# Optimization experiments

Measured on AMD Instinct MI355X. Metric: run time of the kernel, lower is better.

## Reference

```python
import jax, jax.numpy as jnp
import numpy as np


def _round_ste(v):
    # straight-through rounding (typical LinearQuantize autograd STE)
    return v + jax.lax.stop_gradient(jnp.round(v) - v)


def setup_inputs() -> dict:
    key = jax.random.key(0)
    k1, k2, k3 = jax.random.split(key, 3)
    tokens, d_in, d_out = 8192, 2048, 2048
    x = jax.random.uniform(k1, (tokens, d_in), dtype=jnp.float32)  # non-negative acts
    weight = jax.random.normal(k2, (d_out, d_in), dtype=jnp.float32) * 0.02
    bias = jax.random.normal(k3, (d_out,), dtype=jnp.float32) * 0.02
    return {"x": x, "weight": weight, "bias": bias, "weight_bit": 8}


def reference(x, weight, bias, weight_bit):
    n = 2 ** weight_bit
    # stats computed on detached data (x.data/w.data in torch)
    wd = jax.lax.stop_gradient(weight)
    w_min = wd.min(axis=1)                      # [out]
    w_max = wd.max(axis=1)                      # [out]
    x_max = jax.lax.stop_gradient(x).max()
    scale_x = (n - 1) / jnp.clip(x_max, 1e-8)
    # activation quantization: round(scale_x * x - 0)
    q_x = _round_ste(scale_x * x)               # [T, in]
    # per-channel asymmetric weight quant (quantize_int)
    scale_w = (n - 1) / jnp.clip(w_max - w_min, 1e-8)   # [out]
    zp_w = scale_w * w_min                      # [out]
    q_w = _round_ste(scale_w[:, None] * weight - zp_w[:, None])  # [out, in]
    # bias quantized with combined scale, then clamped
    q_b = jnp.clip(_round_ste(bias * scale_w * scale_x), -n - 1, n)  # [out]
    # fake-int GEMM + zero-point correction + rescale
    mult = jnp.einsum('ti,oi->to', q_x, q_w) + q_b      # [T, out]
    res = mult + zp_w * q_x.sum(-1, keepdims=True)
    return res / scale_x / scale_w
```

## Files before the change

### kernel.cpp

```cpp
#include <hip/hip_runtime.h>
#include <stdint.h>

typedef __attribute__((ext_vector_type(4))) int i32x4;

__device__ inline float wave_max(float v){ for(int o=32;o;o>>=1) v=fmaxf(v,__shfl_xor(v,o)); return v; }
__device__ inline float wave_min(float v){ for(int o=32;o;o>>=1) v=fminf(v,__shfl_xor(v,o)); return v; }
__device__ inline int   wave_sum(int v){ for(int o=32;o;o>>=1) v+=__shfl_xor(v,o); return v; }

__device__ inline void gload16(const void* g, void* l){
  __builtin_amdgcn_global_load_lds((const __attribute__((address_space(1))) char*)g,
                                   (__attribute__((address_space(3))) char*)l, 16, 0, 0);
}

__global__ void k_xmax_partial(const float* __restrict__ x, long long n4,
                               float* __restrict__ partials){
  long long i = (long long)blockIdx.x*blockDim.x + threadIdx.x;
  long long stride = (long long)gridDim.x*blockDim.x;
  const float4* x4 = (const float4*)x;
  float m = 0.f;
  for(; i < n4; i += stride){
    float4 v = x4[i];
    m = fmaxf(m, fmaxf(fmaxf(v.x,v.y),fmaxf(v.z,v.w)));
  }
  m = wave_max(m);
  __shared__ float sm[4];
  int lane = threadIdx.x & 63, wid = threadIdx.x >> 6;
  if(lane==0) sm[wid] = m;
  __syncthreads();
  if(threadIdx.x==0)
    partials[blockIdx.x] = fmaxf(fmaxf(sm[0],sm[1]),fmaxf(sm[2],sm[3]));
}

__global__ void k_xmax_final(const float* __restrict__ partials, int nPart,
                             uint32_t* __restrict__ xmax_bits){
  float m = 0.f;
  for(int i = threadIdx.x; i < nPart; i += 256) m = fmaxf(m, partials[i]);
  m = wave_max(m);
  __shared__ float sm[4];
  int lane = threadIdx.x & 63, wid = threadIdx.x >> 6;
  if(lane==0) sm[wid] = m;
  __syncthreads();
  if(threadIdx.x==0)
    *xmax_bits = __float_as_uint(fmaxf(fmaxf(sm[0],sm[1]),fmaxf(sm[2],sm[3])));
}

__global__ void k_wstat(const float* __restrict__ w, const float* __restrict__ bias,
                        const int* __restrict__ wbit, const uint32_t* __restrict__ xmax_bits,
                        float* __restrict__ scale_w, float* __restrict__ zp_w,
                        float* __restrict__ winv,
                        int* __restrict__ cint, char* __restrict__ qw, int din){
  int row = blockIdx.x, tid = threadIdx.x;
  int lane = tid & 63, wid = tid >> 6;
  const float4* wr4 = (const float4*)(w + (long long)row*din);
  float4 a = wr4[tid*2], b = wr4[tid*2+1];
  float v[8] = {a.x,a.y,a.z,a.w,b.x,b.y,b.z,b.w};
  float mn = v[0], mx = v[0];
  for(int j=1;j<8;j++){ mn=fminf(mn,v[j]); mx=fmaxf(mx,v[j]); }
  float wmn = wave_min(mn), wmx = wave_max(mx);
  __shared__ float smn[4], smx[4];
  __shared__ float s_sw, s_zp; __shared__ int s_qb;
  if(lane==0){ smn[wid]=wmn; smx[wid]=wmx; }
  __syncthreads();
  if(tid==0){
    float fmn = fminf(fminf(smn[0],smn[1]),fminf(smn[2],smn[3]));
    float fmx = fmaxf(fmaxf(smx[0],smx[1]),fmaxf(smx[2],smx[3]));
    int n = 1 << *wbit;
    float nm1 = (float)(n-1);
    float xmax = __uint_as_float(*xmax_bits);
    float sx = __fdiv_rn(nm1, fmaxf(xmax, 1e-8f));
    float rng = __fsub_rn(fmx, fmn);
    float rngc = fmaxf(rng, 1e-8f);
    float sw = __fdiv_rn(nm1, rngc);
    float zp = __fmul_rn(sw, fmn);
    float qbf = rintf(__fmul_rn(__fmul_rn(bias[row], sw), sx));
    qbf = fminf(fmaxf(qbf, -(float)(n+1)), (float)n);
    s_sw = sw; s_zp = zp; s_qb = (int)qbf;
    scale_w[row] = sw; zp_w[row] = zp;
    winv[row] = __fdiv_rn(rngc, nm1);
  }
  __syncthreads();
  float sw = s_sw, zp = s_zp;
  int qsum = 0; uint32_t lo = 0, hi = 0;
  for(int j=0;j<8;j++){
    int q = (int)rintf(__fsub_rn(__fmul_rn(sw, v[j]), zp));
    qsum += q;
    uint32_t u = (uint32_t)((q - 128) & 0xff);
    if(j<4) lo |= u << (8*j); else hi |= u << (8*(j-4));
  }
  uint32_t* qrow = (uint32_t*)(qw + (long long)row*din);
  qrow[tid*2] = lo; qrow[tid*2+1] = hi;
  int wsum = wave_sum(qsum);
  __shared__ int ssum[4];
  if(lane==0) ssum[wid] = wsum;
  __syncthreads();
  if(tid==0){
    int Sb = ssum[0]+ssum[1]+ssum[2]+ssum[3];
    cint[row] = 128*Sb - 128*128*din + s_qb;
  }
}

__global__ void k_xquant(const float* __restrict__ x, const int* __restrict__ wbit,
                         const uint32_t* __restrict__ xmax_bits,
                         char* __restrict__ qx, int* __restrict__ Sa, int din){
  int row = blockIdx.x, tid = threadIdx.x;
  int lane = tid & 63, wid = tid >> 6;
  int n = 1 << *wbit;
  float nm1 = (float)(n-1);
  float sx = __fdiv_rn(nm1, fmaxf(__uint_as_float(*xmax_bits), 1e-8f));
  const float4* xr4 = (const float4*)(x + (long long)row*din);
  float4 a = xr4[tid*2], b = xr4[tid*2+1];
  float v[8] = {a.x,a.y,a.z,a.w,b.x,b.y,b.z,b.w};
  int qsum = 0; uint32_t lo = 0, hi = 0;
  for(int j=0;j<8;j++){
    int q = (int)rintf(__fmul_rn(sx, v[j]));
    qsum += q;
    uint32_t u = (uint32_t)((q - 128) & 0xff);
    if(j<4) lo |= u << (8*j); else hi |= u << (8*(j-4));
  }
  uint32_t* qrow = (uint32_t*)(qx + (long long)row*din);
  qrow[tid*2] = lo; qrow[tid*2+1] = hi;
  int wsum = wave_sum(qsum);
  __shared__ int ssum[4];
  if(lane==0) ssum[wid] = wsum;
  __syncthreads();
  if(tid==0) Sa[row] = ssum[0]+ssum[1]+ssum[2]+ssum[3];
}

#define ASLOT 16384
#define BSLOT 8192
#define SLOT  (ASLOT + BSLOT)

__global__ __launch_bounds__(256, 2) void k_gemm(
    const char* __restrict__ qx, const char* __restrict__ qw,
    const int* __restrict__ Sa, const int* __restrict__ cint,
    const float* __restrict__ winv, const float* __restrict__ zp_w,
    const int* __restrict__ wbit, const uint32_t* __restrict__ xmax_bits,
    float* __restrict__ out, int T, int dout, int din){
  extern __shared__ char lds[];
  const int tid = threadIdx.x, lane = tid & 63, wid = tid >> 6;
  const int wr = (wid >> 1) * 128, wc = (wid & 1) * 64;
  const int tileN = blockIdx.x, tileM = blockIdx.y;

  const int rbase = tid >> 2, c2 = tid & 3;
  const char* aG[4]; const char* bG[2]; int ldA[4], ldB[2];
  #pragma unroll
  for(int j=0;j<4;j++){
    int row = j*64 + rbase;
    int sc = c2 ^ ((row >> 1) & 3);
    aG[j] = qx + ((long long)tileM*256 + row)*din + sc*16;
    ldA[j] = (j*256 + tid)*16;
  }
  #pragma unroll
  for(int j=0;j<2;j++){
    int row = j*64 + rbase;
    int sc = c2 ^ ((row >> 1) & 3);
    bG[j] = qw + ((long long)tileN*128 + row)*din + sc*16;
    ldB[j] = ASLOT + (j*256 + tid)*16;
  }

  const int physo = (((lane >> 4) ^ ((lane >> 1) & 3)) * 16);
  const int arowL = wr + (lane & 15);
  const int browL = wc + (lane & 15);

  i32x4 acc[8][4] = {};
  const int nk = din / 64;

  {
    char* s0 = lds; char* s1 = lds + SLOT;
    #pragma unroll
    for(int j=0;j<4;j++) gload16(aG[j], s0 + ldA[j]);
    #pragma unroll
    for(int j=0;j<2;j++) gload16(bG[j], s0 + ldB[j]);
    #pragma unroll
    for(int j=0;j<4;j++) gload16(aG[j] + 64, s1 + ldA[j]);
    #pragma unroll
    for(int j=0;j<2;j++) gload16(bG[j] + 64, s1 + ldB[j]);
  }
  asm volatile("s_waitcnt vmcnt(6)" ::: "memory");
  __builtin_amdgcn_s_barrier();

  for(int kt = 0; kt < nk; ++kt){
    char* As = lds + (kt % 3)*SLOT;
    char* Bs = As + ASLOT;

    if(kt + 2 < nk){
      char* Sn = lds + ((kt + 2) % 3)*SLOT;
      const long long ko = (long long)(kt + 2) * 64;
      #pragma unroll
      for(int j=0;j<4;j++) gload16(aG[j] + ko, Sn + ldA[j]);
      #pragma unroll
      for(int j=0;j<2;j++) gload16(bG[j] + ko, Sn + ldB[j]);
    }

    i32x4 bf[4], af[8];
    #pragma unroll
    for(int ni=0; ni<4; ++ni) bf[ni] = *(const i32x4*)(Bs + (browL + ni*16)*64 + physo);
    #pragma unroll
    for(int mi=0; mi<8; ++mi) af[mi] = *(const i32x4*)(As + (arowL + mi*16)*64 + physo);

    __builtin_amdgcn_s_setprio(1);
    #pragma unroll
    for(int mi=0; mi<8; ++mi)
      #pragma unroll
      for(int ni=0; ni<4; ++ni)
        acc[mi][ni] = __builtin_amdgcn_mfma_i32_16x16x64_i8(af[mi], bf[ni], acc[mi][ni], 0, 0, 0);
    __builtin_amdgcn_s_setprio(0);

    if(kt < nk - 2) asm volatile("s_waitcnt vmcnt(6)" ::: "memory");
    else            asm volatile("s_waitcnt vmcnt(0)" ::: "memory");
    __builtin_amdgcn_s_barrier();
  }

  const float nm1 = (float)((1 << *wbit) - 1);
  const float xmaxc = fmaxf(__uint_as_float(*xmax_bits), 1e-8f);
  const float inv_sx = __fdiv_rn(xmaxc, nm1);
  const int colL = tileN*128 + wc + (lane & 15);
  const int rowL = tileM*256 + wr + ((lane >> 4) * 4);
  float invc[4], zp4[4]; int ci4[4];
  #pragma unroll
  for(int ni=0; ni<4; ++ni){
    int o = colL + ni*16;
    invc[ni] = __fmul_rn(winv[o], inv_sx);
    zp4[ni]  = zp_w[o];
    ci4[ni]  = cint[o];
  }
  #pragma unroll
  for(int mi=0; mi<8; ++mi){
    int rb = rowL + mi*16;
    int sav[4];
    #pragma unroll
    for(int r=0; r<4; ++r) sav[r] = Sa[rb + r];
    #pragma unroll
    for(int ni=0; ni<4; ++ni){
      #pragma unroll
      for(int r=0; r<4; ++r){
        int iv = acc[mi][ni][r] + 128*sav[r] + ci4[ni];
        float f = (float)iv + zp4[ni]*(float)sav[r];
        out[(long long)(rb + r)*dout + colL + ni*16] = __fmul_rn(f, invc[ni]);
      }
    }
  }
}

extern "C" void kernel_launch(void* const* d_in, const int* in_sizes, int n_in,
                              void* d_out, int out_size, void* d_ws, size_t ws_size,
                              hipStream_t stream){
  const float* x    = (const float*)d_in[0];
  const float* w    = (const float*)d_in[1];
  const float* bias = (const float*)d_in[2];
  const int*   wbit = (const int*)d_in[3];
  int dout = in_sizes[2];
  int din  = in_sizes[1] / dout;
  int T    = in_sizes[0] / din;

  const int NPART = 2048;
  char* ws = (char*)d_ws;
  uint32_t* xmax_bits = (uint32_t*)ws;
  size_t off = 256;
  float* partials = (float*)(ws + off); off += 4*(size_t)NPART;
  float* scale_w = (float*)(ws + off); off += 4*(size_t)dout;
  float* zp_w    = (float*)(ws + off); off += 4*(size_t)dout;
  float* winv    = (float*)(ws + off); off += 4*(size_t)dout;
  int*   cint    = (int*)(ws + off);   off += 4*(size_t)dout;
  int*   Sa      = (int*)(ws + off);   off += 4*(size_t)T;
  off = (off + 255) & ~(size_t)255;
  char*  qw      = ws + off;           off += (size_t)dout*din;
  char*  qx      = ws + off;           off += (size_t)T*din;

  long long n4 = (long long)T*din/4;
  k_xmax_partial<<<NPART, 256, 0, stream>>>(x, n4, partials);
  k_xmax_final<<<1, 256, 0, stream>>>(partials, NPART, xmax_bits);
  k_wstat<<<dout, 256, 0, stream>>>(w, bias, wbit, xmax_bits, scale_w, zp_w, winv, cint, qw, din);
  k_xquant<<<T, 256, 0, stream>>>(x, wbit, xmax_bits, qx, Sa, din);
  dim3 grid(dout/128, T/256);
  k_gemm<<<grid, 256, 3*SLOT, stream>>>(qx, qw, Sa, cint, winv, zp_w, wbit, xmax_bits,
                                        (float*)d_out, T, dout, din);
}
```

Baseline: 82.03 us.

## Fuse activation max and quantization with grid barrier; restructure int8 GEMM tiling

Merges the two-pass activation max reduction and the activation quantization into one kernel. Each block keeps its rows in registers and waits on an atomic-counter grid barrier for the global max, so the input is read once instead of twice. The bias quantization moves from the weight-stats kernel into the GEMM epilogue. The GEMM changes to 128x256 tiles: weights are loaded straight into registers, and only the activation tile is staged in a double-buffered LDS buffer, with no swizzle and no async global-to-LDS loads. The spin barrier needs every block to be co-resident, so it risks deadlock, and the unswizzled LDS reads and uncoalesced B loads may slow the GEMM.

```diff
diff --git a/kernel.cpp b/kernel.cpp
--- a/kernel.cpp
+++ b/kernel.cpp
@@ -7,45 +7,62 @@
 __device__ inline float wave_min(float v){ for(int o=32;o;o>>=1) v=fminf(v,__shfl_xor(v,o)); return v; }
 __device__ inline int   wave_sum(int v){ for(int o=32;o;o>>=1) v+=__shfl_xor(v,o); return v; }
 
-__device__ inline void gload16(const void* g, void* l){
-  __builtin_amdgcn_global_load_lds((const __attribute__((address_space(1))) char*)g,
-                                   (__attribute__((address_space(3))) char*)l, 16, 0, 0);
-}
-
-__global__ void k_xmax_partial(const float* __restrict__ x, long long n4,
-                               float* __restrict__ partials){
-  long long i = (long long)blockIdx.x*blockDim.x + threadIdx.x;
-  long long stride = (long long)gridDim.x*blockDim.x;
-  const float4* x4 = (const float4*)x;
+__global__ __launch_bounds__(256, 4) void k_fused_quant(
+    const float* __restrict__ x, const int* __restrict__ wbit,
+    float* __restrict__ partials, uint32_t* __restrict__ cnt,
+    uint32_t* __restrict__ xmax_bits,
+    char* __restrict__ qx, int* __restrict__ Sa, int din, int nblocks){
+  const int tid = threadIdx.x;
+  const int r8 = tid >> 5, c32 = tid & 31;
+  const long long row = (long long)blockIdx.x*8 + r8;
+  const float4* xr = (const float4*)(x + row*din);
+  float4 v[16];
+  #pragma unroll
+  for(int j=0;j<16;j++) v[j] = xr[c32 + j*32];
   float m = 0.f;
-  for(; i < n4; i += stride){
-    float4 v = x4[i];
-    m = fmaxf(m, fmaxf(fmaxf(v.x,v.y),fmaxf(v.z,v.w)));
-  }
+  #pragma unroll
+  for(int j=0;j<16;j++) m = fmaxf(m, fmaxf(fmaxf(v[j].x,v[j].y),fmaxf(v[j].z,v[j].w)));
   m = wave_max(m);
   __shared__ float sm[4];
-  int lane = threadIdx.x & 63, wid = threadIdx.x >> 6;
-  if(lane==0) sm[wid] = m;
-  __syncthreads();
-  if(threadIdx.x==0)
-    partials[blockIdx.x] = fmaxf(fmaxf(sm[0],sm[1]),fmaxf(sm[2],sm[3]));
-}
-
-__global__ void k_xmax_final(const float* __restrict__ partials, int nPart,
-                             uint32_t* __restrict__ xmax_bits){
-  float m = 0.f;
-  for(int i = threadIdx.x; i < nPart; i += 256) m = fmaxf(m, partials[i]);
-  m = wave_max(m);
-  __shared__ float sm[4];
-  int lane = threadIdx.x & 63, wid = threadIdx.x >> 6;
-  if(lane==0) sm[wid] = m;
-  __syncthreads();
-  if(threadIdx.x==0)
-    *xmax_bits = __float_as_uint(fmaxf(fmaxf(sm[0],sm[1]),fmaxf(sm[2],sm[3])));
-}
-
-__global__ void k_wstat(const float* __restrict__ w, const float* __restrict__ bias,
-                        const int* __restrict__ wbit, const uint32_t* __restrict__ xmax_bits,
+  if((tid&63)==0) sm[tid>>6] = m;
+  __syncthreads();
+  if(tid==0){
+    float bm = fmaxf(fmaxf(sm[0],sm[1]),fmaxf(sm[2],sm[3]));
+    partials[blockIdx.x] = bm;
+    __threadfence();
+    __hip_atomic_fetch_add(cnt, 1u, __ATOMIC_RELEASE, __HIP_MEMORY_SCOPE_AGENT);
+    while(__hip_atomic_load(cnt, __ATOMIC_ACQUIRE, __HIP_MEMORY_SCOPE_AGENT) < (uint32_t)nblocks)
+      __builtin_amdgcn_s_sleep(8);
+  }
+  __syncthreads();
+  float mm = 0.f;
+  for(int i=tid;i<nblocks;i+=256) mm = fmaxf(mm, partials[i]);
+  mm = wave_max(mm);
+  if((tid&63)==0) sm[tid>>6] = mm;
+  __syncthreads();
+  const float xmax = fmaxf(fmaxf(sm[0],sm[1]),fmaxf(sm[2],sm[3]));
+  if(tid==0 && blockIdx.x==0) *xmax_bits = __float_as_uint(xmax);
+  const int n = 1 << *wbit;
+  const float sx = __fdiv_rn((float)(n-1), fmaxf(xmax, 1e-8f));
+  uint32_t* qrow = (uint32_t*)(qx + row*din);
+  int qsum = 0;
+  #pragma unroll
+  for(int j=0;j<16;j++){
+    int q0 = (int)rintf(__fmul_rn(sx, v[j].x));
+    int q1 = (int)rintf(__fmul_rn(sx, v[j].y));
+    int q2 = (int)rintf(__fmul_rn(sx, v[j].z));
+    int q3 = (int)rintf(__fmul_rn(sx, v[j].w));
+    qsum += q0+q1+q2+q3;
+    uint32_t pk = ((uint32_t)((q0-128)&0xff)) | ((uint32_t)((q1-128)&0xff)<<8) |
+                  ((uint32_t)((q2-128)&0xff)<<16) | ((uint32_t)((q3-128)&0xff)<<24);
+    qrow[c32 + j*32] = pk;
+  }
+  for(int o=16;o;o>>=1) qsum += __shfl_xor(qsum, o);
+  if(c32==0) Sa[row] = qsum;
+}
+
+__global__ void k_wstat(const float* __restrict__ w,
+                        const int* __restrict__ wbit,
                         float* __restrict__ scale_w, float* __restrict__ zp_w,
                         float* __restrict__ winv,
                         int* __restrict__ cint, char* __restrict__ qw, int din){
@@ -58,7 +75,7 @@
   for(int j=1;j<8;j++){ mn=fminf(mn,v[j]); mx=fmaxf(mx,v[j]); }
   float wmn = wave_min(mn), wmx = wave_max(mx);
   __shared__ float smn[4], smx[4];
-  __shared__ float s_sw, s_zp; __shared__ int s_qb;
+  __shared__ float s_sw, s_zp;
   if(lane==0){ smn[wid]=wmn; smx[wid]=wmx; }
   __syncthreads();
   if(tid==0){
@@ -66,15 +83,10 @@
     float fmx = fmaxf(fmaxf(smx[0],smx[1]),fmaxf(smx[2],smx[3]));
     int n = 1 << *wbit;
     float nm1 = (float)(n-1);
-    float xmax = __uint_as_float(*xmax_bits);
-    float sx = __fdiv_rn(nm1, fmaxf(xmax, 1e-8f));
-    float rng = __fsub_rn(fmx, fmn);
-    float rngc = fmaxf(rng, 1e-8f);
+    float rngc = fmaxf(__fsub_rn(fmx, fmn), 1e-8f);
     float sw = __fdiv_rn(nm1, rngc);
     float zp = __fmul_rn(sw, fmn);
-    float qbf = rintf(__fmul_rn(__fmul_rn(bias[row], sw), sx));
-    qbf = fminf(fmaxf(qbf, -(float)(n+1)), (float)n);
-    s_sw = sw; s_zp = zp; s_qb = (int)qbf;
+    s_sw = sw; s_zp = zp;
     scale_w[row] = sw; zp_w[row] = zp;
     winv[row] = __fdiv_rn(rngc, nm1);
   }
@@ -95,134 +107,97 @@
   __syncthreads();
   if(tid==0){
     int Sb = ssum[0]+ssum[1]+ssum[2]+ssum[3];
-    cint[row] = 128*Sb - 128*128*din + s_qb;
-  }
-}
-
-__global__ void k_xquant(const float* __restrict__ x, const int* __restrict__ wbit,
-                         const uint32_t* __restrict__ xmax_bits,
-                         char* __restrict__ qx, int* __restrict__ Sa, int din){
-  int row = blockIdx.x, tid = threadIdx.x;
-  int lane = tid & 63, wid = tid >> 6;
-  int n = 1 << *wbit;
-  float nm1 = (float)(n-1);
-  float sx = __fdiv_rn(nm1, fmaxf(__uint_as_float(*xmax_bits), 1e-8f));
-  const float4* xr4 = (const float4*)(x + (long long)row*din);
-  float4 a = xr4[tid*2], b = xr4[tid*2+1];
-  float v[8] = {a.x,a.y,a.z,a.w,b.x,b.y,b.z,b.w};
-  int qsum = 0; uint32_t lo = 0, hi = 0;
-  for(int j=0;j<8;j++){
-    int q = (int)rintf(__fmul_rn(sx, v[j]));
-    qsum += q;
-    uint32_t u = (uint32_t)((q - 128) & 0xff);
-    if(j<4) lo |= u << (8*j); else hi |= u << (8*(j-4));
-  }
-  uint32_t* qrow = (uint32_t*)(qx + (long long)row*din);
-  qrow[tid*2] = lo; qrow[tid*2+1] = hi;
-  int wsum = wave_sum(qsum);
-  __shared__ int ssum[4];
-  if(lane==0) ssum[wid] = wsum;
-  __syncthreads();
-  if(tid==0) Sa[row] = ssum[0]+ssum[1]+ssum[2]+ssum[3];
-}
-
-#define ASLOT 16384
-#define BSLOT 8192
-#define SLOT  (ASLOT + BSLOT)
+    cint[row] = 128*Sb - 128*128*din;
+  }
+}
 
 __global__ __launch_bounds__(256, 2) void k_gemm(
     const char* __restrict__ qx, const char* __restrict__ qw,
     const int* __restrict__ Sa, const int* __restrict__ cint,
-    const float* __restrict__ winv, const float* __restrict__ zp_w,
+    const float* __restrict__ scale_w, const float* __restrict__ winv,
+    const float* __restrict__ zp_w, const float* __restrict__ bias,
     const int* __restrict__ wbit, const uint32_t* __restrict__ xmax_bits,
     float* __restrict__ out, int T, int dout, int din){
-  extern __shared__ char lds[];
+  __shared__ __align__(16) char Abuf[2][8192];
   const int tid = threadIdx.x, lane = tid & 63, wid = tid >> 6;
-  const int wr = (wid >> 1) * 128, wc = (wid & 1) * 64;
   const int tileN = blockIdx.x, tileM = blockIdx.y;
-
-  const int rbase = tid >> 2, c2 = tid & 3;
-  const char* aG[4]; const char* bG[2]; int ldA[4], ldB[2];
-  #pragma unroll
-  for(int j=0;j<4;j++){
-    int row = j*64 + rbase;
-    int sc = c2 ^ ((row >> 1) & 3);
-    aG[j] = qx + ((long long)tileM*256 + row)*din + sc*16;
-    ldA[j] = (j*256 + tid)*16;
-  }
-  #pragma unroll
-  for(int j=0;j<2;j++){
-    int row = j*64 + rbase;
-    int sc = c2 ^ ((row >> 1) & 3);
-    bG[j] = qw + ((long long)tileN*128 + row)*din + sc*16;
-    ldB[j] = ASLOT + (j*256 + tid)*16;
-  }
-
-  const int physo = (((lane >> 4) ^ ((lane >> 1) & 3)) * 16);
-  const int arowL = wr + (lane & 15);
-  const int browL = wc + (lane & 15);
+  const int nk = din / 64;
+
+  const char* aSrc0 = qx + ((long long)tileM*128 + (tid>>2))*din + (tid&3)*16;
+  const char* aSrc1 = aSrc0 + (long long)64*din;
+  const int aLds = tid*16;
+
+  const char* bBase = qw + ((long long)tileN*256 + wid*64 + (lane&15))*din + (lane>>4)*16;
+  const long long bNi = (long long)16*din;
+
+  const int aRd = (lane&15)*64 + (lane>>4)*16;
 
   i32x4 acc[8][4] = {};
-  const int nk = din / 64;
-
-  {
-    char* s0 = lds; char* s1 = lds + SLOT;
-    #pragma unroll
-    for(int j=0;j<4;j++) gload16(aG[j], s0 + ldA[j]);
-    #pragma unroll
-    for(int j=0;j<2;j++) gload16(bG[j], s0 + ldB[j]);
-    #pragma unroll
-    for(int j=0;j<4;j++) gload16(aG[j] + 64, s1 + ldA[j]);
-    #pragma unroll
-    for(int j=0;j<2;j++) gload16(bG[j] + 64, s1 + ldB[j]);
-  }
-  asm volatile("s_waitcnt vmcnt(6)" ::: "memory");
+  i32x4 aR0, aR1, aN0, aN1, bR[4], bN[4];
+
+  aR0 = *(const i32x4*)(aSrc0);
+  aR1 = *(const i32x4*)(aSrc1);
+  *(i32x4*)(&Abuf[0][aLds])        = aR0;
+  *(i32x4*)(&Abuf[0][aLds + 4096]) = aR1;
+  aR0 = *(const i32x4*)(aSrc0 + 64);
+  aR1 = *(const i32x4*)(aSrc1 + 64);
+  #pragma unroll
+  for(int ni=0; ni<4; ++ni) bR[ni] = *(const i32x4*)(bBase + ni*bNi);
+  asm volatile("s_waitcnt lgkmcnt(0)" ::: "memory");
   __builtin_amdgcn_s_barrier();
 
-  for(int kt = 0; kt < nk; ++kt){
-    char* As = lds + (kt % 3)*SLOT;
-    char* Bs = As + ASLOT;
-
-    if(kt + 2 < nk){
-      char* Sn = lds + ((kt + 2) % 3)*SLOT;
-      const long long ko = (long long)(kt + 2) * 64;
-      #pragma unroll
-      for(int j=0;j<4;j++) gload16(aG[j] + ko, Sn + ldA[j]);
-      #pragma unroll
-      for(int j=0;j<2;j++) gload16(bG[j] + ko, Sn + ldB[j]);
-    }
-
-    i32x4 bf[4], af[8];
-    #pragma unroll
-    for(int ni=0; ni<4; ++ni) bf[ni] = *(const i32x4*)(Bs + (browL + ni*16)*64 + physo);
-    #pragma unroll
-    for(int mi=0; mi<8; ++mi) af[mi] = *(const i32x4*)(As + (arowL + mi*16)*64 + physo);
+  for(int t = 0; t < nk; ++t){
+    const bool ldA = (t + 2 < nk), ldB = (t + 1 < nk);
+    if(ldA){
+      aN0 = *(const i32x4*)(aSrc0 + (long long)(t+2)*64);
+      aN1 = *(const i32x4*)(aSrc1 + (long long)(t+2)*64);
+    }
+    if(ldB){
+      #pragma unroll
+      for(int ni=0; ni<4; ++ni) bN[ni] = *(const i32x4*)(bBase + ni*bNi + (long long)(t+1)*64);
+    }
+    const char* Ab = Abuf[t & 1];
+    i32x4 af[8];
+    #pragma unroll
+    for(int mi=0; mi<8; ++mi) af[mi] = *(const i32x4*)(Ab + aRd + mi*1024);
 
     __builtin_amdgcn_s_setprio(1);
     #pragma unroll
     for(int mi=0; mi<8; ++mi)
       #pragma unroll
       for(int ni=0; ni<4; ++ni)
-        acc[mi][ni] = __builtin_amdgcn_mfma_i32_16x16x64_i8(af[mi], bf[ni], acc[mi][ni], 0, 0, 0);
+        acc[mi][ni] = __builtin_amdgcn_mfma_i32_16x16x64_i8(af[mi], bR[ni], acc[mi][ni], 0, 0, 0);
     __builtin_amdgcn_s_setprio(0);
 
-    if(kt < nk - 2) asm volatile("s_waitcnt vmcnt(6)" ::: "memory");
-    else            asm volatile("s_waitcnt vmcnt(0)" ::: "memory");
+    if(ldB){
+      char* An = Abuf[(t+1) & 1];
+      *(i32x4*)(An + aLds)        = aR0;
+      *(i32x4*)(An + aLds + 4096) = aR1;
+      aR0 = aN0; aR1 = aN1;
+      #pragma unroll
+      for(int ni=0; ni<4; ++ni) bR[ni] = bN[ni];
+    }
+    asm volatile("s_waitcnt lgkmcnt(0)" ::: "memory");
     __builtin_amdgcn_s_barrier();
   }
 
-  const float nm1 = (float)((1 << *wbit) - 1);
+  const int n = 1 << *wbit;
+  const float nm1 = (float)(n-1);
   const float xmaxc = fmaxf(__uint_as_float(*xmax_bits), 1e-8f);
+  const float sx = __fdiv_rn(nm1, xmaxc);
   const float inv_sx = __fdiv_rn(xmaxc, nm1);
-  const int colL = tileN*128 + wc + (lane & 15);
-  const int rowL = tileM*256 + wr + ((lane >> 4) * 4);
+  const int colL = tileN*256 + wid*64 + (lane & 15);
+  const int rowL = tileM*128 + ((lane >> 4) * 4);
   float invc[4], zp4[4]; int ci4[4];
   #pragma unroll
   for(int ni=0; ni<4; ++ni){
     int o = colL + ni*16;
+    float sw = scale_w[o];
+    float qbf = rintf(__fmul_rn(__fmul_rn(bias[o], sw), sx));
+    qbf = fminf(fmaxf(qbf, -(float)(n+1)), (float)n);
+    ci4[ni] = cint[o] + (int)qbf;
     invc[ni] = __fmul_rn(winv[o], inv_sx);
     zp4[ni]  = zp_w[o];
-    ci4[ni]  = cint[o];
   }
   #pragma unroll
   for(int mi=0; mi<8; ++mi){
@@ -253,11 +228,12 @@
   int din  = in_sizes[1] / dout;
   int T    = in_sizes[0] / din;
 
-  const int NPART = 2048;
   char* ws = (char*)d_ws;
   uint32_t* xmax_bits = (uint32_t*)ws;
+  uint32_t* cnt       = (uint32_t*)(ws + 64);
   size_t off = 256;
-  float* partials = (float*)(ws + off); off += 4*(size_t)NPART;
+  int nQB = T / 8;
+  float* partials = (float*)(ws + off); off += 4*(size_t)nQB;
   float* scale_w = (float*)(ws + off); off += 4*(size_t)dout;
   float* zp_w    = (float*)(ws + off); off += 4*(size_t)dout;
   float* winv    = (float*)(ws + off); off += 4*(size_t)dout;
@@ -267,12 +243,10 @@
   char*  qw      = ws + off;           off += (size_t)dout*din;
   char*  qx      = ws + off;           off += (size_t)T*din;
 
-  long long n4 = (long long)T*din/4;
-  k_xmax_partial<<<NPART, 256, 0, stream>>>(x, n4, partials);
-  k_xmax_final<<<1, 256, 0, stream>>>(partials, NPART, xmax_bits);
-  k_wstat<<<dout, 256, 0, stream>>>(w, bias, wbit, xmax_bits, scale_w, zp_w, winv, cint, qw, din);
-  k_xquant<<<T, 256, 0, stream>>>(x, wbit, xmax_bits, qx, Sa, din);
-  dim3 grid(dout/128, T/256);
-  k_gemm<<<grid, 256, 3*SLOT, stream>>>(qx, qw, Sa, cint, winv, zp_w, wbit, xmax_bits,
-                                        (float*)d_out, T, dout, din);
-}
+  hipMemsetAsync(cnt, 0, 4, stream);
+  k_fused_quant<<<nQB, 256, 0, stream>>>(x, wbit, partials, cnt, xmax_bits, qx, Sa, din, nQB);
+  k_wstat<<<dout, 256, 0, stream>>>(w, wbit, scale_w, zp_w, winv, cint, qw, din);
+  dim3 grid(dout/256, T/128);
+  k_gemm<<<grid, 256, 0, stream>>>(qx, qw, Sa, cint, scale_w, winv, zp_w, bias, wbit, xmax_bits,
+                                   (float*)d_out, T, dout, din);
+}
```

Measured after the change: 218.9 us, median of 2. +166.9%, slower.
